# Kernel tuning notes

Hardware: AMD Instinct MI355X
Metric: run time of the kernel (lower is better)

Reference implementation:

```python
import jax, jax.numpy as jnp
import numpy as np

NV = 100000   # vehicle nodes
NE = 100000   # 'edge' nodes (dst type)
E = 250000    # graph edges (connects relation)
VDIM = 16
EDIM = 16
HID = 128
HEADS = 4
DH = 128      # out_feats per head (GATv2Conv(hid, hid))
EPS = 1e-5
NEG_SLOPE = 0.2


def _layernorm(x, g, b):
    mu = x.mean(-1, keepdims=True)
    var = ((x - mu) ** 2).mean(-1, keepdims=True)
    return (x - mu) * jax.lax.rsqrt(var + EPS) * g + b


def setup_inputs() -> dict:
    key = jax.random.key(0)
    ks = jax.random.split(key, 20)
    s = 0.05
    return {
        "v_feat": jax.random.normal(ks[0], (NV, VDIM), jnp.float32),
        "e_feat": jax.random.normal(ks[1], (NE, EDIM), jnp.float32),
        "Wv": jax.random.normal(ks[2], (VDIM, HID), jnp.float32) * s,
        "bv": jnp.zeros((HID,), jnp.float32),
        "gv": jnp.ones((HID,), jnp.float32),
        "betav": jnp.zeros((HID,), jnp.float32),
        "We": jax.random.normal(ks[3], (EDIM, HID), jnp.float32) * s,
        "be": jnp.zeros((HID,), jnp.float32),
        "ge": jnp.ones((HID,), jnp.float32),
        "betae": jnp.zeros((HID,), jnp.float32),
        "Wsrc": jax.random.normal(ks[4], (HID, HEADS * DH), jnp.float32) * s,
        "bsrc": jnp.zeros((HEADS * DH,), jnp.float32),
        "Wdst": jax.random.normal(ks[5], (HID, HEADS * DH), jnp.float32) * s,
        "bdst": jnp.zeros((HEADS * DH,), jnp.float32),
        "attn": jax.random.normal(ks[6], (HEADS, DH), jnp.float32) * s,
        "Wp": jax.random.normal(ks[7], (HID, HID), jnp.float32) * s,
        "bp": jnp.zeros((HID,), jnp.float32),
        "src": jax.random.randint(ks[8], (E,), 0, NV, jnp.int32),
        "dst": jax.random.randint(ks[9], (E,), 0, NE, jnp.int32),
    }


def reference(v_feat, e_feat, Wv, bv, gv, betav, We, be, ge, betae,
              Wsrc, bsrc, Wdst, bdst, attn, Wp, bp, src, dst):
    # --- node-type encoders: Linear -> ReLU -> LayerNorm ---
    h_v = _layernorm(jax.nn.relu(v_feat @ Wv + bv), gv, betav)      # [NV, HID]
    h_e = _layernorm(jax.nn.relu(e_feat @ We + be), ge, betae)      # [NE, HID]

    # --- GATv2Conv (bipartite: vehicle -> edge), 4 heads ---
    fs = (h_v @ Wsrc + bsrc).reshape(NV, HEADS, DH)                 # src proj
    fd = (h_e @ Wdst + bdst).reshape(NE, HEADS, DH)                 # dst proj
    e = jax.nn.leaky_relu(fs[src] + fd[dst], NEG_SLOPE)             # [E, H, D]
    score = jnp.einsum("ehd,hd->eh", e, attn)                       # [E, H]
    # segment-wise (per-dst-node) softmax over incoming edges
    smax = jax.ops.segment_max(score, dst, num_segments=NE)         # [NE, H]
    ex = jnp.exp(score - smax[dst])
    denom = jax.ops.segment_sum(ex, dst, num_segments=NE)
    alpha = ex / denom[dst]                                         # [E, H]
    out = jax.ops.segment_sum(alpha[:, :, None] * fs[src], dst,
                              num_segments=NE)                      # [NE, H, D]

    # HeteroGraphConv mean-aggregate (single relation -> identity),
    # then mean over heads (edge_out.dim()==3 branch)
    edge_out = out.mean(axis=1)                                     # [NE, HID]

    # feature_proj: Linear -> ReLU -> Dropout(eval: identity)
    return jax.nn.relu(edge_out @ Wp + bp)
```

## Files before the change

kernel.cpp:

```cpp
#include <hip/hip_runtime.h>
#include <hip/hip_bf16.h>
#include <math.h>

#define NV 100000
#define NE_N 100000
#define NEDGE 250000
#define NEG 0.2f
#define LN_EPS 1e-5f

typedef __bf16 bf16_t;
typedef __bf16 bf16x8 __attribute__((ext_vector_type(8)));
typedef float f32x4 __attribute__((ext_vector_type(4)));

__device__ inline unsigned short f2bfu(float f) {
    return __builtin_bit_cast(unsigned short, (__bf16)f);
}
__device__ inline float bfu2f(unsigned short u) {
    return (float)__builtin_bit_cast(__bf16, u);
}
__device__ inline float blo(unsigned w) { return __uint_as_float(w << 16); }
__device__ inline float bhi(unsigned w) { return __uint_as_float(w & 0xffff0000u); }
__device__ inline float lrelu(float x) { return x > 0.f ? x : NEG * x; }
__device__ inline unsigned pk2(float a, float b) {
    return (unsigned)f2bfu(a) | ((unsigned)f2bfu(b) << 16);
}

__global__ __launch_bounds__(256) void prep_kernel(
    const float* __restrict__ Wsrc, const float* __restrict__ Wdst,
    const float* __restrict__ Wp, bf16_t* __restrict__ pS,
    bf16_t* __restrict__ pD, bf16_t* __restrict__ pP)
{
    int t = blockIdx.x * 256 + threadIdx.x;
    if (t < 8192) {
        int ksq = t >> 9, col = t & 511;
#pragma unroll
        for (int j = 0; j < 8; ++j)
            pS[(size_t)t * 8 + j] = (bf16_t)Wsrc[(ksq * 8 + j) * 512 + col];
    } else if (t < 16384) {
        int g = t - 8192;
        int ksq = g >> 9, col = g & 511;
#pragma unroll
        for (int j = 0; j < 8; ++j)
            pD[(size_t)g * 8 + j] = (bf16_t)Wdst[(ksq * 8 + j) * 512 + col];
    } else if (t < 18432) {
        int g = t - 16384;
        int ksq = g >> 7, col = g & 127;
#pragma unroll
        for (int j = 0; j < 8; ++j)
            pP[(size_t)g * 8 + j] = (bf16_t)Wp[(ksq * 8 + j) * 128 + col];
    }
}

__global__ __launch_bounds__(256) void count_kernel(
    const int* __restrict__ dst, int* __restrict__ deg)
{
    int t = blockIdx.x * 256 + threadIdx.x;
    if (t < NEDGE) atomicAdd(&deg[dst[t]], 1);
}

__global__ __launch_bounds__(256) void scan1_kernel(
    const int* __restrict__ deg, int* __restrict__ offs, int* __restrict__ bsum)
{
    __shared__ int s[256];
    int i = blockIdx.x * 256 + threadIdx.x;
    int v = (i < NE_N) ? deg[i] : 0;
    s[threadIdx.x] = v;
    __syncthreads();
    for (int off = 1; off < 256; off <<= 1) {
        int t_ = (threadIdx.x >= off) ? s[threadIdx.x - off] : 0;
        __syncthreads();
        s[threadIdx.x] += t_;
        __syncthreads();
    }
    if (i < NE_N) offs[i] = s[threadIdx.x] - v;
    if (threadIdx.x == 255) bsum[blockIdx.x] = s[255];
}

__global__ __launch_bounds__(512) void scan2_kernel(int* __restrict__ bsum, int nb)
{
    __shared__ int s[512];
    int t = threadIdx.x;
    int v = (t < nb) ? bsum[t] : 0;
    s[t] = v;
    __syncthreads();
    for (int off = 1; off < 512; off <<= 1) {
        int t_ = (t >= off) ? s[t - off] : 0;
        __syncthreads();
        s[t] += t_;
        __syncthreads();
    }
    if (t < nb) bsum[t] = s[t] - v;
}

__global__ __launch_bounds__(256) void scan3_kernel(
    int* __restrict__ offs, const int* __restrict__ bsum, int* __restrict__ cursor)
{
    int i = blockIdx.x * 256 + threadIdx.x;
    if (i < NE_N) {
        int o = offs[i] + bsum[blockIdx.x];
        offs[i] = o;
        cursor[i] = o;
    }
}

__global__ __launch_bounds__(256) void scatter_kernel(
    const int* __restrict__ dst, int* __restrict__ cursor, int* __restrict__ eidx)
{
    int t = blockIdx.x * 256 + threadIdx.x;
    if (t < NEDGE) {
        int pos = atomicAdd(&cursor[dst[t]], 1);
        eidx[pos] = t;
    }
}

__global__ __launch_bounds__(256, 4) void enc_proj_kernel(
    const float* __restrict__ featV, const float* __restrict__ WencV,
    const float* __restrict__ bencV, const float* __restrict__ gV,
    const float* __restrict__ betaV, const bf16_t* __restrict__ ApackV,
    const float* __restrict__ bprojV, unsigned short* __restrict__ outV,
    const float* __restrict__ featE, const float* __restrict__ WencE,
    const float* __restrict__ bencE, const float* __restrict__ gE,
    const float* __restrict__ betaE, const bf16_t* __restrict__ ApackE,
    const float* __restrict__ bprojE, unsigned short* __restrict__ outE,
    int nblk1, int M)
{
    __shared__ unsigned short Hs[64 * 136];

    int b = blockIdx.x;
    bool isV = b < nblk1;
    const float* feat  = isV ? featV  : featE;
    const float* Wenc  = isV ? WencV  : WencE;
    const float* benc  = isV ? bencV  : bencE;
    const float* gln   = isV ? gV     : gE;
    const float* beta  = isV ? betaV  : betaE;
    const bf16_t* Apack = isV ? ApackV : ApackE;
    const float* bproj = isV ? bprojV : bprojE;
    unsigned short* out = isV ? outV : outE;
    int row0 = (isV ? b : b - nblk1) * 64;

    int t = threadIdx.x;
    int l = t & 63;
    int w = t >> 6;
    int rbase = __builtin_amdgcn_readfirstlane(w * 16);

    float wc0[16], wc1[16];
#pragma unroll
    for (int k = 0; k < 16; ++k) {
        float2 wv = *(const float2*)(Wenc + k * 128 + 2 * l);
        wc0[k] = wv.x;
        wc1[k] = wv.y;
    }
    float2 bv2 = *(const float2*)(benc + 2 * l);

#pragma unroll
    for (int i = 0; i < 16; ++i) {
        int grow = row0 + rbase + i;
        if (grow >= M) grow = M - 1;
        const float* fr = feat + (size_t)grow * 16;
        float a0 = bv2.x, a1 = bv2.y;
#pragma unroll
        for (int k = 0; k < 16; ++k) {
            float f = fr[k];
            a0 = fmaf(f, wc0[k], a0);
            a1 = fmaf(f, wc1[k], a1);
        }
        a0 = fmaxf(a0, 0.f);
        a1 = fmaxf(a1, 0.f);
        *(unsigned*)&Hs[(rbase + i) * 136 + 2 * l] = pk2(a0, a1);
    }

    float s = 0.f, s2 = 0.f;
    {
        int rr = rbase + (l >> 2);
        int q = l & 3;
#pragma unroll
        for (int j = 0; j < 4; ++j) {
            uint4 v = *(const uint4*)&Hs[rr * 136 + q * 32 + j * 8];
            float x;
            x = blo(v.x); s += x; s2 = fmaf(x, x, s2);
            x = bhi(v.x); s += x; s2 = fmaf(x, x, s2);
            x = blo(v.y); s += x; s2 = fmaf(x, x, s2);
            x = bhi(v.y); s += x; s2 = fmaf(x, x, s2);
            x = blo(v.z); s += x; s2 = fmaf(x, x, s2);
            x = bhi(v.z); s += x; s2 = fmaf(x, x, s2);
            x = blo(v.w); s += x; s2 = fmaf(x, x, s2);
            x = bhi(v.w); s += x; s2 = fmaf(x, x, s2);
        }
    }
    s  += __shfl_xor(s, 1, 64);  s  += __shfl_xor(s, 2, 64);
    s2 += __shfl_xor(s2, 1, 64); s2 += __shfl_xor(s2, 2, 64);
    float mu  = s * (1.f / 128.f);
    float var = s2 * (1.f / 128.f) - mu * mu;
    float inv = rsqrtf(var + LN_EPS);

    int kq = l >> 4;
    int ln = l & 15;
    float mu_r  = __shfl(mu,  ln * 4, 64);
    float inv_r = __shfl(inv, ln * 4, 64);

    bf16x8 bfr[4];
#pragma unroll
    for (int ks = 0; ks < 4; ++ks) {
        int c0 = ks * 32 + kq * 8;
        uint4 v = *(const uint4*)&Hs[(rbase + ln) * 136 + c0];
        float4 g0 = *(const float4*)(gln + c0);
        float4 g1 = *(const float4*)(gln + c0 + 4);
        float4 b0 = *(const float4*)(beta + c0);
        float4 b1 = *(const float4*)(beta + c0 + 4);
        uint4 p;
        p.x = pk2(fmaf((blo(v.x) - mu_r) * inv_r, g0.x, b0.x),
                  fmaf((bhi(v.x) - mu_r) * inv_r, g0.y, b0.y));
        p.y = pk2(fmaf((blo(v.y) - mu_r) * inv_r, g0.z, b0.z),
                  fmaf((bhi(v.y) - mu_r) * inv_r, g0.w, b0.w));
        p.z = pk2(fmaf((blo(v.z) - mu_r) * inv_r, g1.x, b1.x),
                  fmaf((bhi(v.z) - mu_r) * inv_r, g1.y, b1.y));
        p.w = pk2(fmaf((blo(v.w) - mu_r) * inv_r, g1.z, b1.z),
                  fmaf((bhi(v.w) - mu_r) * inv_r, g1.w, b1.w));
        bfr[ks] = __builtin_bit_cast(bf16x8, p);
    }

    unsigned short* stag = Hs + rbase * 136;
    int node = row0 + rbase + ln;
    bool wr = node < M;

    bf16x8 a_cur[4], a_nxt[4];
#pragma unroll
    for (int ks = 0; ks < 4; ++ks)
        a_cur[ks] = *(const bf16x8*)(Apack + ((size_t)(ks * 4 + kq) * 512 + ln) * 8);

#pragma unroll
    for (int pass = 0; pass < 4; ++pass) {
        int colp = pass * 128;
#pragma unroll
        for (int mt = 0; mt < 8; ++mt) {
            int nidx = pass * 8 + mt + 1;
            if (nidx < 32) {
                int ncol = (nidx >> 3) * 128 + (nidx & 7) * 16 + ln;
#pragma unroll
                for (int ks = 0; ks < 4; ++ks)
                    a_nxt[ks] = *(const bf16x8*)(Apack + ((size_t)(ks * 4 + kq) * 512 + ncol) * 8);
            }

            f32x4 acc = {0.f, 0.f, 0.f, 0.f};
#pragma unroll
            for (int ks = 0; ks < 4; ++ks)
                acc = __builtin_amdgcn_mfma_f32_16x16x32_bf16(a_cur[ks], bfr[ks], acc, 0, 0, 0);

            int col = colp + mt * 16 + kq * 4;
            float4 bb = *(const float4*)(bproj + col);
            ushort4 o;
            o.x = f2bfu(acc[0] + bb.x);
            o.y = f2bfu(acc[1] + bb.y);
            o.z = f2bfu(acc[2] + bb.z);
            o.w = f2bfu(acc[3] + bb.w);
            *(ushort4*)&stag[ln * 136 + mt * 16 + kq * 4] = o;

#pragma unroll
            for (int ks = 0; ks < 4; ++ks)
                a_cur[ks] = a_nxt[ks];
        }
#pragma unroll
        for (int i = 0; i < 4; ++i) {
            uint4 v = *(const uint4*)&stag[ln * 136 + i * 32 + kq * 8];
            if (wr)
                *(uint4*)(out + (size_t)node * 512 + colp + i * 32 + kq * 8) = v;
        }
    }
}

__global__ __launch_bounds__(256) void final_gemm_kernel(
    const float* __restrict__ A, const bf16_t* __restrict__ Ppack,
    const float* __restrict__ bp, float* __restrict__ C, int M)
{
    __shared__ unsigned short Hs[64 * 136];
    int t = threadIdx.x;
    int lane = t & 63;
    int w = t >> 6;
    int row0 = blockIdx.x * 64;

#pragma unroll
    for (int i = 0; i < 8; ++i) {
        int f4 = i * 256 + t;
        int r = f4 >> 5;
        int c4 = (f4 & 31) * 4;
        float4 v = make_float4(0.f, 0.f, 0.f, 0.f);
        if (row0 + r < M)
            v = ((const float4*)(A + (size_t)(row0 + r) * 128))[f4 & 31];
        ushort4 o;
        o.x = f2bfu(v.x); o.y = f2bfu(v.y); o.z = f2bfu(v.z); o.w = f2bfu(v.w);
        *(ushort4*)&Hs[r * 136 + c4] = o;
    }
    __syncthreads();

    int kq = lane >> 4;
    int ln = lane & 15;

    f32x4 acc[2][4];
#pragma unroll
    for (int mt = 0; mt < 2; ++mt)
#pragma unroll
        for (int nt = 0; nt < 4; ++nt) {
            f32x4 z = {0.f, 0.f, 0.f, 0.f};
            acc[mt][nt] = z;
        }

#pragma unroll
    for (int ks = 0; ks < 4; ++ks) {
        bf16x8 bfr[4];
#pragma unroll
        for (int nt = 0; nt < 4; ++nt) {
            const uint4* p = (const uint4*)&Hs[(nt * 16 + ln) * 136 + ks * 32 + kq * 8];
            bfr[nt] = __builtin_bit_cast(bf16x8, *p);
        }
        bf16x8 afr[2];
#pragma unroll
        for (int mt = 0; mt < 2; ++mt) {
            int colA = w * 32 + mt * 16 + ln;
            afr[mt] = *(const bf16x8*)(Ppack + ((size_t)(ks * 4 + kq) * 128 + colA) * 8);
        }
#pragma unroll
        for (int mt = 0; mt < 2; ++mt)
#pragma unroll
            for (int nt = 0; nt < 4; ++nt)
                acc[mt][nt] = __builtin_amdgcn_mfma_f32_16x16x32_bf16(
                    afr[mt], bfr[nt], acc[mt][nt], 0, 0, 0);
    }

#pragma unroll
    for (int mt = 0; mt < 2; ++mt) {
        int col = w * 32 + mt * 16 + kq * 4;
        float4 bb = *(const float4*)(bp + col);
#pragma unroll
        for (int nt = 0; nt < 4; ++nt) {
            int node = row0 + nt * 16 + ln;
            if (node < M) {
                float4 o;
                o.x = fmaxf(acc[mt][nt][0] + bb.x, 0.f);
                o.y = fmaxf(acc[mt][nt][1] + bb.y, 0.f);
                o.z = fmaxf(acc[mt][nt][2] + bb.z, 0.f);
                o.w = fmaxf(acc[mt][nt][3] + bb.w, 0.f);
                *(float4*)(C + (size_t)node * 128 + col) = o;
            }
        }
    }
}

__global__ __launch_bounds__(256) void softagg_kernel(
    const unsigned short* __restrict__ fs, const unsigned short* __restrict__ fdp,
    const float* __restrict__ attn, const int* __restrict__ src,
    const int* __restrict__ offs, const int* __restrict__ deg,
    const int* __restrict__ eidx, float* __restrict__ out)
{
    int d = blockIdx.x * 4 + (threadIdx.x >> 6);
    if (d >= NE_N) return;
    int l = threadIdx.x & 63;
    int r0 = offs[d];
    int n = deg[d];
    int o = l * 8;

    uint4 fv = *(const uint4*)(fdp + (size_t)d * 512 + o);
    float fdv[8] = { blo(fv.x), bhi(fv.x), blo(fv.y), bhi(fv.y),
                     blo(fv.z), bhi(fv.z), blo(fv.w), bhi(fv.w) };
    float4 w0 = *(const float4*)(attn + o);
    float4 w1 = *(const float4*)(attn + o + 4);
    float wv[8] = { w0.x, w0.y, w0.z, w0.w, w1.x, w1.y, w1.z, w1.w };

    float m = -1e30f, sm = 0.f;
    float acc[8];
#pragma unroll
    for (int j = 0; j < 8; ++j) acc[j] = 0.f;

    for (int base = 0; base < n; base += 64) {
        int cnt = min(n - base, 64);
        int sl = 0;
        if (l < cnt) sl = src[eidx[r0 + base + l]];
        for (int i = 0; i < cnt; ++i) {
            int s = __shfl(sl, i, 64);
            uint4 a = *(const uint4*)(fs + (size_t)s * 512 + o);
            float fsv[8] = { blo(a.x), bhi(a.x), blo(a.y), bhi(a.y),
                             blo(a.z), bhi(a.z), blo(a.w), bhi(a.w) };
            float p = 0.f;
#pragma unroll
            for (int j = 0; j < 8; ++j)
                p = fmaf(lrelu(fsv[j] + fdv[j]), wv[j], p);
#pragma unroll
            for (int mk = 1; mk < 16; mk <<= 1)
                p += __shfl_xor(p, mk, 64);
            float mn = fmaxf(m, p);
            float c  = __expf(m - mn);
            float av = __expf(p - mn);
            sm = sm * c + av;
            m = mn;
#pragma unroll
            for (int j = 0; j < 8; ++j)
                acc[j] = fmaf(av, fsv[j], acc[j] * c);
        }
    }

    float inv = (n > 0) ? 0.25f / sm : 0.f;
#pragma unroll
    for (int j = 0; j < 8; ++j) {
        float v = acc[j] * inv;
        v += __shfl_xor(v, 16, 64);
        v += __shfl_xor(v, 32, 64);
        acc[j] = v;
    }
    if (l < 16) {
        float4 o0 = make_float4(acc[0], acc[1], acc[2], acc[3]);
        float4 o1 = make_float4(acc[4], acc[5], acc[6], acc[7]);
        *(float4*)(out + (size_t)d * 128 + l * 8) = o0;
        *(float4*)(out + (size_t)d * 128 + l * 8 + 4) = o1;
    }
}

extern "C" void kernel_launch(void* const* d_in, const int* in_sizes, int n_in,
                              void* d_out, int out_size, void* d_ws, size_t ws_size,
                              hipStream_t stream)
{
    const float* v_feat = (const float*)d_in[0];
    const float* e_feat = (const float*)d_in[1];
    const float* Wv     = (const float*)d_in[2];
    const float* bv     = (const float*)d_in[3];
    const float* gv     = (const float*)d_in[4];
    const float* betav  = (const float*)d_in[5];
    const float* We     = (const float*)d_in[6];
    const float* be     = (const float*)d_in[7];
    const float* ge     = (const float*)d_in[8];
    const float* betae  = (const float*)d_in[9];
    const float* Wsrc   = (const float*)d_in[10];
    const float* bsrc   = (const float*)d_in[11];
    const float* Wdst   = (const float*)d_in[12];
    const float* bdst   = (const float*)d_in[13];
    const float* attn   = (const float*)d_in[14];
    const float* Wp     = (const float*)d_in[15];
    const float* bp     = (const float*)d_in[16];
    const int*   src    = (const int*)d_in[17];
    const int*   dst    = (const int*)d_in[18];
    float* out = (float*)d_out;

    unsigned short* fs = (unsigned short*)d_ws;
    unsigned short* fd = fs + (size_t)NV * 512;
    int* deg    = (int*)(fd + (size_t)NE_N * 512);
    int* offs   = deg + NE_N;
    int* cursor = offs + NE_N;
    int* bsum   = cursor + NE_N;
    int* eidx   = bsum + 512;
    bf16_t* pS  = (bf16_t*)(eidx + NEDGE);
    bf16_t* pD  = pS + 65536;
    bf16_t* pP  = pD + 65536;

    const int NB_SCAN = (NE_N + 255) / 256;

    prep_kernel<<<72, 256, 0, stream>>>(Wsrc, Wdst, Wp, pS, pD, pP);

    hipMemsetAsync(deg, 0, (size_t)NE_N * sizeof(int), stream);
    count_kernel<<<(NEDGE + 255) / 256, 256, 0, stream>>>(dst, deg);
    scan1_kernel<<<NB_SCAN, 256, 0, stream>>>(deg, offs, bsum);
    scan2_kernel<<<1, 512, 0, stream>>>(bsum, NB_SCAN);
    scan3_kernel<<<NB_SCAN, 256, 0, stream>>>(offs, bsum, cursor);
    scatter_kernel<<<(NEDGE + 255) / 256, 256, 0, stream>>>(dst, cursor, eidx);

    enc_proj_kernel<<<3126, 256, 0, stream>>>(
        v_feat, Wv, bv, gv, betav, pS, bsrc, fs,
        e_feat, We, be, ge, betae, pD, bdst, fd,
        1563, 100000);

    softagg_kernel<<<NE_N / 4, 256, 0, stream>>>(fs, fd, attn, src, offs, deg,
                                                 eidx, out);

    final_gemm_kernel<<<1563, 256, 0, stream>>>(out, pP, bp, out, NE_N);
}
```

Before: 330.9 us.

## Stage projection weights through LDS with async double-buffering; batch gather loads

The encoder-projection kernel now streams the packed bf16 weight tiles into shared memory using global_load_lds into a double buffer, with waitcnt and barriers. Each wave reads its MFMA operands from LDS instead of having every wave fetch them from global memory, and the bias also comes from LDS. Separately, the attention aggregation loop issues four source-feature gathers before processing them, to raise memory-level parallelism. The cost is more LDS (about 34KB per block), which may lower occupancy, plus a barrier per pass.

```diff
diff --git a/kernel.cpp b/kernel.cpp
--- a/kernel.cpp
+++ b/kernel.cpp
@@ -23,6 +23,13 @@
 __device__ inline float lrelu(float x) { return x > 0.f ? x : NEG * x; }
 __device__ inline unsigned pk2(float a, float b) {
     return (unsigned)f2bfu(a) | ((unsigned)f2bfu(b) << 16);
+}
+
+__device__ __forceinline__ void gload_lds16(const bf16_t* g, unsigned short* l) {
+    __builtin_amdgcn_global_load_lds(
+        (const __attribute__((address_space(1))) unsigned int*)g,
+        (__attribute__((address_space(3))) unsigned int*)l,
+        16, 0, 0);
 }
 
 __global__ __launch_bounds__(256) void prep_kernel(
@@ -125,6 +132,8 @@
     int nblk1, int M)
 {
     __shared__ unsigned short Hs[64 * 136];
+    __shared__ __align__(16) unsigned short Abuf[2][8192];
+    __shared__ __align__(16) float Bias[512];
 
     int b = blockIdx.x;
     bool isV = b < nblk1;
@@ -142,6 +151,14 @@
     int l = t & 63;
     int w = t >> 6;
     int rbase = __builtin_amdgcn_readfirstlane(w * 16);
+
+#pragma unroll
+    for (int j = 0; j < 4; ++j) {
+        int ksq = w * 4 + j;
+        gload_lds16(Apack + ((size_t)(ksq * 512) + l) * 8, &Abuf[0][ksq * 512]);
+    }
+    if (t < 128)
+        *(float4*)&Bias[t * 4] = *(const float4*)(bproj + t * 4);
 
     float wc0[16], wc1[16];
 #pragma unroll
@@ -223,47 +240,51 @@
     int node = row0 + rbase + ln;
     bool wr = node < M;
 
-    bf16x8 a_cur[4], a_nxt[4];
-#pragma unroll
-    for (int ks = 0; ks < 4; ++ks)
-        a_cur[ks] = *(const bf16x8*)(Apack + ((size_t)(ks * 4 + kq) * 512 + ln) * 8);
-
-#pragma unroll
-    for (int pass = 0; pass < 4; ++pass) {
-        int colp = pass * 128;
-#pragma unroll
-        for (int mt = 0; mt < 8; ++mt) {
-            int nidx = pass * 8 + mt + 1;
-            if (nidx < 32) {
-                int ncol = (nidx >> 3) * 128 + (nidx & 7) * 16 + ln;
-#pragma unroll
-                for (int ks = 0; ks < 4; ++ks)
-                    a_nxt[ks] = *(const bf16x8*)(Apack + ((size_t)(ks * 4 + kq) * 512 + ncol) * 8);
+#pragma unroll
+    for (int p = 0; p < 8; ++p) {
+        if (p == 0)
+            asm volatile("s_waitcnt vmcnt(0) lgkmcnt(0)" ::: "memory");
+        else
+            asm volatile("s_waitcnt vmcnt(2)" ::: "memory");
+        __builtin_amdgcn_s_barrier();
+
+        if (p < 7) {
+#pragma unroll
+            for (int j = 0; j < 4; ++j) {
+                int ksq = w * 4 + j;
+                gload_lds16(Apack + ((size_t)(ksq * 512 + (p + 1) * 64) + l) * 8,
+                            &Abuf[(p + 1) & 1][ksq * 512]);
             }
+            __builtin_amdgcn_sched_barrier(0);
+        }
+
+        const unsigned short* Ac = Abuf[p & 1];
+#pragma unroll
+        for (int mt = 0; mt < 4; ++mt) {
+            bf16x8 a[4];
+#pragma unroll
+            for (int ks = 0; ks < 4; ++ks)
+                a[ks] = *(const bf16x8*)&Ac[((ks * 4 + kq) * 64 + mt * 16 + ln) * 8];
 
             f32x4 acc = {0.f, 0.f, 0.f, 0.f};
 #pragma unroll
             for (int ks = 0; ks < 4; ++ks)
-                acc = __builtin_amdgcn_mfma_f32_16x16x32_bf16(a_cur[ks], bfr[ks], acc, 0, 0, 0);
-
-            int col = colp + mt * 16 + kq * 4;
-            float4 bb = *(const float4*)(bproj + col);
+                acc = __builtin_amdgcn_mfma_f32_16x16x32_bf16(a[ks], bfr[ks], acc, 0, 0, 0);
+
+            int colp = p * 64 + mt * 16 + kq * 4;
+            float4 bb = *(const float4*)&Bias[colp];
             ushort4 o;
             o.x = f2bfu(acc[0] + bb.x);
             o.y = f2bfu(acc[1] + bb.y);
             o.z = f2bfu(acc[2] + bb.z);
             o.w = f2bfu(acc[3] + bb.w);
             *(ushort4*)&stag[ln * 136 + mt * 16 + kq * 4] = o;
-
-#pragma unroll
-            for (int ks = 0; ks < 4; ++ks)
-                a_cur[ks] = a_nxt[ks];
-        }
-#pragma unroll
-        for (int i = 0; i < 4; ++i) {
+        }
+#pragma unroll
+        for (int i = 0; i < 2; ++i) {
             uint4 v = *(const uint4*)&stag[ln * 136 + i * 32 + kq * 8];
             if (wr)
-                *(uint4*)(out + (size_t)node * 512 + colp + i * 32 + kq * 8) = v;
+                *(uint4*)(out + (size_t)node * 512 + p * 64 + i * 32 + kq * 8) = v;
         }
     }
 }
@@ -374,26 +395,39 @@
         int cnt = min(n - base, 64);
         int sl = 0;
         if (l < cnt) sl = src[eidx[r0 + base + l]];
-        for (int i = 0; i < cnt; ++i) {
-            int s = __shfl(sl, i, 64);
-            uint4 a = *(const uint4*)(fs + (size_t)s * 512 + o);
-            float fsv[8] = { blo(a.x), bhi(a.x), blo(a.y), bhi(a.y),
-                             blo(a.z), bhi(a.z), blo(a.w), bhi(a.w) };
-            float p = 0.f;
-#pragma unroll
-            for (int j = 0; j < 8; ++j)
-                p = fmaf(lrelu(fsv[j] + fdv[j]), wv[j], p);
-#pragma unroll
-            for (int mk = 1; mk < 16; mk <<= 1)
-                p += __shfl_xor(p, mk, 64);
-            float mn = fmaxf(m, p);
-            float c  = __expf(m - mn);
-            float av = __expf(p - mn);
-            sm = sm * c + av;
-            m = mn;
-#pragma unroll
-            for (int j = 0; j < 8; ++j)
-                acc[j] = fmaf(av, fsv[j], acc[j] * c);
+        for (int i0 = 0; i0 < cnt; i0 += 4) {
+            uint4 av[4];
+#pragma unroll
+            for (int j = 0; j < 4; ++j) {
+                int idx = (i0 + j < cnt) ? i0 + j : cnt - 1;
+                int s = __shfl(sl, idx, 64);
+                av[j] = *(const uint4*)(fs + (size_t)s * 512 + o);
+            }
+            int mcnt = min(4, cnt - i0);
+#pragma unroll
+            for (int j = 0; j < 4; ++j) {
+                if (j < mcnt) {
+                    float fsv[8] = { blo(av[j].x), bhi(av[j].x),
+                                     blo(av[j].y), bhi(av[j].y),
+                                     blo(av[j].z), bhi(av[j].z),
+                                     blo(av[j].w), bhi(av[j].w) };
+                    float p = 0.f;
+#pragma unroll
+                    for (int jj = 0; jj < 8; ++jj)
+                        p = fmaf(lrelu(fsv[jj] + fdv[jj]), wv[jj], p);
+#pragma unroll
+                    for (int mk = 1; mk < 16; mk <<= 1)
+                        p += __shfl_xor(p, mk, 64);
+                    float mn = fmaxf(m, p);
+                    float c  = __expf(m - mn);
+                    float aw = __expf(p - mn);
+                    sm = sm * c + aw;
+                    m = mn;
+#pragma unroll
+                    for (int jj = 0; jj < 8; ++jj)
+                        acc[jj] = fmaf(aw, fsv[jj], acc[jj] * c);
+                }
+            }
         }
     }
 
```

Result: no change. 336.6 us (+1.7%).
